# Kernel optimization log

Measured on AMD Instinct MI355X. Metric: run time of the kernel, lower is better.

Reference implementation:

```python
import jax, jax.numpy as jnp
import numpy as np

EMBED_DIM = 1024
NUM_HEADS = 16
HEAD_DIM = EMBED_DIM // NUM_HEADS
ROPE_BASE = 10000.0


def setup_inputs() -> dict:
    key = jax.random.key(0)
    k1, k2, k3, k4, k5 = jax.random.split(key, 5)
    b, t = 4, 2048
    s = 1.0 / np.sqrt(EMBED_DIM)
    return {
        "query": jax.random.normal(k1, (b, t, EMBED_DIM), jnp.float32),
        "in_proj_w": jax.random.normal(k2, (3 * EMBED_DIM, EMBED_DIM), jnp.float32) * s,
        "in_proj_b": jax.random.normal(k3, (3 * EMBED_DIM,), jnp.float32) * 0.02,
        "out_proj_w": jax.random.normal(k4, (EMBED_DIM, EMBED_DIM), jnp.float32) * s,
        "out_proj_b": jax.random.normal(k5, (EMBED_DIM,), jnp.float32) * 0.02,
    }


def _rope_cos_sin(t: int, dtype):
    inv_freq = 1.0 / (ROPE_BASE ** (jnp.arange(0, HEAD_DIM, 2, dtype=jnp.float32) / HEAD_DIM))
    freqs = jnp.arange(t, dtype=jnp.float32)[:, None] * inv_freq[None, :]  # [t, hd/2]
    return jnp.cos(freqs).astype(dtype), jnp.sin(freqs).astype(dtype)


def _apply_rotary(x, cos, sin):
    # x: [b, h, t, hd]; cos/sin: [t, hd/2]
    x1 = x[..., ::2]
    x2 = x[..., 1::2]
    c = cos[None, None, :, :]
    s = sin[None, None, :, :]
    rotated = jnp.stack((x1 * c - x2 * s, x1 * s + x2 * c), axis=-1)  # [b,h,t,hd/2,2]
    return rotated.reshape(x.shape)


def reference(query, in_proj_w, in_proj_b, out_proj_w, out_proj_b):
    b, t, d = query.shape
    qkv = query @ in_proj_w.T + in_proj_b  # [b, t, 3d]
    q, k, v = jnp.split(qkv, 3, axis=-1)
    def heads(x):
        return x.reshape(b, t, NUM_HEADS, HEAD_DIM).transpose(0, 2, 1, 3)  # [b,h,t,hd]
    q, k, v = heads(q), heads(k), heads(v)
    cos, sin = _rope_cos_sin(t, query.dtype)
    q = _apply_rotary(q, cos, sin)
    k = _apply_rotary(k, cos, sin)
    scale = 1.0 / np.sqrt(HEAD_DIM)
    scores = jnp.einsum('bhqd,bhkd->bhqk', q, k) * scale  # [b,h,t,t]
    probs = jax.nn.softmax(scores, axis=-1)
    attn = jnp.einsum('bhqk,bhkd->bhqd', probs, v)
    out = attn.transpose(0, 2, 1, 3).reshape(b, t, d)
    return out @ out_proj_w.T + out_proj_b
```

## Files before the change

kernel.cpp:

```cpp
#include <hip/hip_runtime.h>
#include <hip/hip_bf16.h>

#define EMBED 1024
#define NHEADS 16
#define HDIM 64
#define BATCH 4
#define SEQ 2048
#define BT (BATCH*SEQ)
#define NQKV (3*EMBED)


typedef _Float16 f16;
typedef __attribute__((ext_vector_type(8))) _Float16 half8;
typedef __attribute__((ext_vector_type(4))) _Float16 half4;
typedef __attribute__((ext_vector_type(4))) float f32x4;
typedef __attribute__((ext_vector_type(16))) float f32x16;
typedef __attribute__((ext_vector_type(4))) unsigned int u32x4;

__device__ __forceinline__ f32x4 mfma16f(half8 a, half8 b, f32x4 c) {
    return __builtin_amdgcn_mfma_f32_16x16x32_f16(a, b, c, 0, 0, 0);
}
__device__ __forceinline__ f32x16 mfma32(half8 a, half8 b, f32x16 c) {
    return __builtin_amdgcn_mfma_f32_32x32x16_f16(a, b, c, 0, 0, 0);
}
__device__ __forceinline__ f32x16 z16() {
    f32x16 z;
    #pragma unroll
    for (int i = 0; i < 16; i++) z[i] = 0.f;
    return z;
}
__device__ __forceinline__ unsigned int pk16(float a, float b) {
    auto h = __builtin_amdgcn_cvt_pkrtz(a, b);
    return __builtin_bit_cast(unsigned int, h);
}
__device__ __forceinline__ half8 mk8(unsigned int w0, unsigned int w1,
                                     unsigned int w2, unsigned int w3) {
    u32x4 v = (u32x4){w0, w1, w2, w3};
    return __builtin_bit_cast(half8, v);
}
__device__ __forceinline__ void pswap(unsigned int &a, unsigned int &b) {
    asm("v_permlane32_swap_b32 %0, %1" : "+v"(a), "+v"(b));
}

__device__ __forceinline__ half8 cvt8(float4 a, float4 b) {
    half8 r;
    r[0] = (f16)a.x; r[1] = (f16)a.y; r[2] = (f16)a.z; r[3] = (f16)a.w;
    r[4] = (f16)b.x; r[5] = (f16)b.y; r[6] = (f16)b.z; r[7] = (f16)b.w;
    return r;
}

__device__ __forceinline__ void gload16(const void* g, void* l) {
    __builtin_amdgcn_global_load_lds(
        (const __attribute__((address_space(1))) void*)g,
        (__attribute__((address_space(3))) void*)l, 16, 0, 0);
}

__global__ __launch_bounds__(256) void cvt_kernel(
    const float* __restrict__ X, const float* __restrict__ W1,
    const float* __restrict__ W2, f16* __restrict__ Xh,
    f16* __restrict__ W1h, f16* __restrict__ W2h, float2* __restrict__ CSt)
{
    const int u0 = blockIdx.x * 256 + threadIdx.x;
    #pragma unroll
    for (int i = 0; i < 3; i++) {
        const size_t uu = (size_t)u0 + (size_t)i * 524288;
        const float* src; f16* dst; size_t off;
        if (uu < 1048576)      { src = X;  dst = Xh;  off = uu * 8; }
        else if (uu < 1441792) { src = W1; dst = W1h; off = (uu - 1048576) * 8; }
        else                   { src = W2; dst = W2h; off = (uu - 1441792) * 8; }
        float4 a = *(const float4*)(src + off);
        float4 b = *(const float4*)(src + off + 4);
        *(half8*)(dst + off) = cvt8(a, b);
    }
    if (u0 < SEQ * 32) {
        const int t = u0 >> 5, fi = u0 & 31;
        const float ang = (float)t * exp2f(-0.41524103f * (float)fi);
        CSt[u0] = make_float2(cosf(ang), sinf(ang));
    }
}

__global__ __launch_bounds__(256) void qkv_rope_kernel(
    const f16* __restrict__ Xh, const f16* __restrict__ Wh,
    const float* __restrict__ bias, const float2* __restrict__ CSt,
    f16* __restrict__ Qg, f16* __restrict__ Kg, f16* __restrict__ Vtg)
{
    __shared__ __align__(16) char smem[34816];
    f16* Ah = (f16*)smem;
    f16* Bh = (f16*)(smem + 16384);
    f16 (*Ep)[136] = (f16(*)[136])smem;

    const int tid = threadIdx.x;
    const int m0 = blockIdx.y * 128, n0 = blockIdx.x * 128;
    const int lane = tid & 63;
    const int wv = tid >> 6, wm = wv >> 1, wn = wv & 1;
    const int quad = lane >> 4, l15 = lane & 15;
    const int sw = (l15 & 7) << 4;

    const int srow  = tid >> 3;
    const int sslot = (tid & 7) ^ (srow & 7);
    const f16* asrc = Xh + (size_t)(m0 + srow) * EMBED + sslot * 8;
    const f16* bsrc = Wh + (size_t)(n0 + srow) * EMBED + sslot * 8;

    f32x4 acc[4][4];
    #pragma unroll
    for (int i = 0; i < 4; i++)
        #pragma unroll
        for (int j = 0; j < 4; j++) acc[i][j] = (f32x4){0.f,0.f,0.f,0.f};

    for (int k0 = 0; k0 < EMBED; k0 += 64) {
        #pragma unroll
        for (int i = 0; i < 4; i++) {
            gload16(asrc + (size_t)i*32*EMBED + k0, Ah + i*2048 + tid*8);
            gload16(bsrc + (size_t)i*32*EMBED + k0, Bh + i*2048 + tid*8);
        }
        __syncthreads();

        half8 bf[4][2];
        #pragma unroll
        for (int nj = 0; nj < 4; nj++) {
            const int rb = wn*64 + nj*16 + l15;
            bf[nj][0] = *(const half8*)((const char*)Bh + rb*128 + ((quad*16) ^ sw));
            bf[nj][1] = *(const half8*)((const char*)Bh + rb*128 + ((64 + quad*16) ^ sw));
        }
        #pragma unroll
        for (int mi = 0; mi < 4; mi++) {
            const int ra = wm*64 + mi*16 + l15;
            half8 a0 = *(const half8*)((const char*)Ah + ra*128 + ((quad*16) ^ sw));
            half8 a1 = *(const half8*)((const char*)Ah + ra*128 + ((64 + quad*16) ^ sw));
            #pragma unroll
            for (int nj = 0; nj < 4; nj++) {
                acc[mi][nj] = mfma16f(a0, bf[nj][0], acc[mi][nj]);
                acc[mi][nj] = mfma16f(a1, bf[nj][1], acc[mi][nj]);
            }
        }
        __syncthreads();
    }

    const int sect = n0 >> 10;
    const int h0   = (n0 & 1023) >> 6;
    const int bb   = m0 >> 11, t0 = m0 & 2047;

    #pragma unroll
    for (int mi = 0; mi < 4; mi++) {
        #pragma unroll
        for (int nj = 0; nj < 4; nj++) {
            const int ncol = wn*64 + nj*16 + l15;
            const int hd = ncol & 63;
            const float bz = bias[n0 + ncol];
            #pragma unroll
            for (int r = 0; r < 4; r++) {
                const int tl = wm*64 + mi*16 + quad*4 + r;
                float v = acc[mi][nj][r] + bz;
                if (sect < 2) {
                    float partner = __shfl_xor(v, 1, 64);
                    float2 cs2 = CSt[(t0 + tl)*32 + (hd >> 1)];
                    float o = (hd & 1) ? fmaf(partner, cs2.y, v * cs2.x)
                                       : fmaf(v, cs2.x, -(partner * cs2.y));
                    Ep[tl][ncol] = (f16)o;
                } else {
                    Ep[ncol][tl] = (f16)v;
                }
            }
        }
    }
    __syncthreads();

    const int orow = tid >> 1;
    const int oc   = (tid & 1) * 64;
    f16* dst;
    if (sect == 2) {
        const int h = h0 + (orow >> 6), d = orow & 63;
        dst = Vtg + ((size_t)((bb*NHEADS + h) * HDIM + d)) * SEQ + t0 + oc;
    } else {
        const int h = h0 + (tid & 1);
        f16* base = (sect == 0) ? Qg : Kg;
        dst = base + ((size_t)((bb*NHEADS + h) * SEQ + t0 + orow)) * HDIM;
    }
    #pragma unroll
    for (int c8 = 0; c8 < 8; c8++)
        *(half8*)(dst + c8*8) = *(const half8*)&Ep[orow][oc + c8*8];
}

__global__ __launch_bounds__(128, 2) void attn_kernel(
    const f16* __restrict__ Qg, const f16* __restrict__ Kg,
    const f16* __restrict__ Vtg, f16* __restrict__ Ow)
{
    __shared__ __align__(16) f16 KV[2][2][64*64];

    const int tid  = threadIdx.x;
    const int lane = tid & 63, wq = tid >> 6;
    const int hi   = lane >> 5, col = lane & 31;

    const int lin = blockIdx.y * 16 + blockIdx.x;
    const int bh  = (lin & 7) + ((lin >> 7) << 3);
    const int qb  = (lin >> 3) & 15;
    const int q0  = qb * 128;

    const f16* Kb = Kg  + (size_t)bh * SEQ * HDIM;
    const f16* Vb = Vtg + (size_t)bh * HDIM * SEQ;

    const int r8   = tid >> 3;
    const int slot = tid & 7;

    #pragma unroll
    for (int g = 0; g < 4; g++) {
        const int row = g*16 + r8;
        const int sc  = (slot ^ (row & 7)) * 8;
        gload16(Kb + (size_t)row * HDIM + sc, &KV[0][0][0] + g*1024 + tid*8);
        gload16(Vb + (size_t)row * SEQ  + sc, &KV[0][1][0] + g*1024 + tid*8);
    }

    half8 qf[2][4];
    #pragma unroll
    for (int nb = 0; nb < 2; nb++) {
        const f16* qsrc = Qg + (size_t)bh * SEQ * HDIM
                        + (size_t)(q0 + wq*64 + nb*32 + col) * HDIM + hi*8;
        #pragma unroll
        for (int kc = 0; kc < 4; kc++)
            qf[nb][kc] = *(const half8*)(qsrc + kc*16);
    }

    f32x16 oacc[2][2];
    oacc[0][0] = z16(); oacc[0][1] = z16();
    oacc[1][0] = z16(); oacc[1][1] = z16();
    float lsum[2] = {0.f, 0.f};

    __syncthreads();

    for (int it = 0; it < 32; it++) {
        const f16* kl = &KV[it & 1][0][0];
        const f16* vl = &KV[it & 1][1][0];

        if (it < 31) {
            f16* kd = &KV[(it + 1) & 1][0][0];
            f16* vd = &KV[(it + 1) & 1][1][0];
            const int j0n = (it + 1) * 64;
            #pragma unroll
            for (int g = 0; g < 4; g++) {
                const int row = g*16 + r8;
                const int sc  = (slot ^ (row & 7)) * 8;
                gload16(Kb + (size_t)(j0n + row) * HDIM + sc, kd + g*1024 + tid*8);
                gload16(Vb + (size_t)row * SEQ + j0n + sc,    vd + g*1024 + tid*8);
            }
        }

        half8 kf[2][4];
        #pragma unroll
        for (int jb = 0; jb < 2; jb++) {
            const int row = jb*32 + col;
            const char* base = (const char*)kl + row*128;
            const int sz = (row & 7) << 4;
            #pragma unroll
            for (int kc = 0; kc < 4; kc++)
                kf[jb][kc] = *(const half8*)(base + ((kc*32 + hi*16) ^ sz));
        }

        unsigned int pw[2][4][4];
        #pragma unroll
        for (int nb = 0; nb < 2; nb++) {
            f32x16 s0 = z16(), s1 = z16();
            __builtin_amdgcn_s_setprio(1);
            #pragma unroll
            for (int kc = 0; kc < 4; kc++) s0 = mfma32(kf[0][kc], qf[nb][kc], s0);
            #pragma unroll
            for (int kc = 0; kc < 4; kc++) s1 = mfma32(kf[1][kc], qf[nb][kc], s1);
            __builtin_amdgcn_s_setprio(0);

            float e0[16], e1[16];
            #pragma unroll
            for (int r = 0; r < 16; r++) {
                e0[r] = __expf(fmaf(s0[r], 0.125f, -4.0f));
                e1[r] = __expf(fmaf(s1[r], 0.125f, -4.0f));
            }
            float t00 = (e0[0]+e0[1]) + (e0[2]+e0[3]);
            float t01 = (e0[4]+e0[5]) + (e0[6]+e0[7]);
            float t02 = (e0[8]+e0[9]) + (e0[10]+e0[11]);
            float t03 = (e0[12]+e0[13]) + (e0[14]+e0[15]);
            float t10 = (e1[0]+e1[1]) + (e1[2]+e1[3]);
            float t11 = (e1[4]+e1[5]) + (e1[6]+e1[7]);
            float t12 = (e1[8]+e1[9]) + (e1[10]+e1[11]);
            float t13 = (e1[12]+e1[13]) + (e1[14]+e1[15]);
            lsum[nb] += ((t00+t01)+(t02+t03)) + ((t10+t11)+(t12+t13));

            unsigned int a, b;
            a = pk16(e0[0],  e0[1]);  b = pk16(e0[4],  e0[5]);
            pswap(a, b); pw[nb][0][0] = a; pw[nb][0][2] = b;
            a = pk16(e0[2],  e0[3]);  b = pk16(e0[6],  e0[7]);
            pswap(a, b); pw[nb][0][1] = a; pw[nb][0][3] = b;
            a = pk16(e0[8],  e0[9]);  b = pk16(e0[12], e0[13]);
            pswap(a, b); pw[nb][1][0] = a; pw[nb][1][2] = b;
            a = pk16(e0[10], e0[11]); b = pk16(e0[14], e0[15]);
            pswap(a, b); pw[nb][1][1] = a; pw[nb][1][3] = b;

            a = pk16(e1[0],  e1[1]);  b = pk16(e1[4],  e1[5]);
            pswap(a, b); pw[nb][2][0] = a; pw[nb][2][2] = b;
            a = pk16(e1[2],  e1[3]);  b = pk16(e1[6],  e1[7]);
            pswap(a, b); pw[nb][2][1] = a; pw[nb][2][3] = b;
            a = pk16(e1[8],  e1[9]);  b = pk16(e1[12], e1[13]);
            pswap(a, b); pw[nb][3][0] = a; pw[nb][3][2] = b;
            a = pk16(e1[10], e1[11]); b = pk16(e1[14], e1[15]);
            pswap(a, b); pw[nb][3][1] = a; pw[nb][3][3] = b;
        }

        __builtin_amdgcn_s_setprio(1);
        #pragma unroll
        for (int kc2 = 0; kc2 < 4; kc2++) {
            half8 pb0 = mk8(pw[0][kc2][0], pw[0][kc2][1], pw[0][kc2][2], pw[0][kc2][3]);
            half8 pb1 = mk8(pw[1][kc2][0], pw[1][kc2][1], pw[1][kc2][2], pw[1][kc2][3]);
            #pragma unroll
            for (int db = 0; db < 2; db++) {
                const int row = db*32 + col;
                const int sz = (row & 7) << 4;
                half8 vf = *(const half8*)((const char*)vl + row*128
                                           + ((kc2*32 + hi*16) ^ sz));
                oacc[db][0] = mfma32(vf, pb0, oacc[db][0]);
                oacc[db][1] = mfma32(vf, pb1, oacc[db][1]);
            }
        }
        __builtin_amdgcn_s_setprio(0);

        __syncthreads();
    }

    float invl[2];
    invl[0] = 1.0f / (lsum[0] + __shfl_xor(lsum[0], 32, 64));
    invl[1] = 1.0f / (lsum[1] + __shfl_xor(lsum[1], 32, 64));

    const int bb = bh >> 4, h = bh & 15;
    #pragma unroll
    for (int nb = 0; nb < 2; nb++) {
        const int t = q0 + wq*64 + nb*32 + col;
        f16* od = Ow + (size_t)(bb*SEQ + t) * EMBED + h*HDIM + hi*4;
        #pragma unroll
        for (int db = 0; db < 2; db++) {
            #pragma unroll
            for (int rg = 0; rg < 4; rg++) {
                half4 o;
                o[0] = (f16)(oacc[db][nb][rg*4+0] * invl[nb]);
                o[1] = (f16)(oacc[db][nb][rg*4+1] * invl[nb]);
                o[2] = (f16)(oacc[db][nb][rg*4+2] * invl[nb]);
                o[3] = (f16)(oacc[db][nb][rg*4+3] * invl[nb]);
                *(half4*)(od + db*32 + rg*8) = o;
            }
        }
    }
}

__global__ __launch_bounds__(256) void outproj_kernel(
    const f16* __restrict__ Aw, const f16* __restrict__ Wh,
    const float* __restrict__ bias, float* __restrict__ Out)
{
    __shared__ __align__(16) char smem[32768];
    f16* Ah = (f16*)smem;
    f16* Bh = (f16*)(smem + 16384);

    const int tid = threadIdx.x;
    const int m0 = blockIdx.y * 128, n0 = blockIdx.x * 128;
    const int lane = tid & 63;
    const int wv = tid >> 6, wm = wv >> 1, wn = wv & 1;
    const int quad = lane >> 4, l15 = lane & 15;
    const int sw = (l15 & 7) << 4;

    const int srow  = tid >> 3;
    const int sslot = (tid & 7) ^ (srow & 7);
    const f16* asrc = Aw + (size_t)(m0 + srow) * EMBED + sslot * 8;
    const f16* bsrc = Wh + (size_t)(n0 + srow) * EMBED + sslot * 8;

    f32x4 acc[4][4];
    #pragma unroll
    for (int i = 0; i < 4; i++)
        #pragma unroll
        for (int j = 0; j < 4; j++) acc[i][j] = (f32x4){0.f,0.f,0.f,0.f};

    for (int k0 = 0; k0 < EMBED; k0 += 64) {
        #pragma unroll
        for (int i = 0; i < 4; i++) {
            gload16(asrc + (size_t)i*32*EMBED + k0, Ah + i*2048 + tid*8);
            gload16(bsrc + (size_t)i*32*EMBED + k0, Bh + i*2048 + tid*8);
        }
        __syncthreads();

        half8 bf[4][2];
        #pragma unroll
        for (int nj = 0; nj < 4; nj++) {
            const int rb = wn*64 + nj*16 + l15;
            bf[nj][0] = *(const half8*)((const char*)Bh + rb*128 + ((quad*16) ^ sw));
            bf[nj][1] = *(const half8*)((const char*)Bh + rb*128 + ((64 + quad*16) ^ sw));
        }
        #pragma unroll
        for (int mi = 0; mi < 4; mi++) {
            const int ra = wm*64 + mi*16 + l15;
            half8 a0 = *(const half8*)((const char*)Ah + ra*128 + ((quad*16) ^ sw));
            half8 a1 = *(const half8*)((const char*)Ah + ra*128 + ((64 + quad*16) ^ sw));
            #pragma unroll
            for (int nj = 0; nj < 4; nj++) {
                acc[mi][nj] = mfma16f(a0, bf[nj][0], acc[mi][nj]);
                acc[mi][nj] = mfma16f(a1, bf[nj][1], acc[mi][nj]);
            }
        }
        __syncthreads();
    }

    #pragma unroll
    for (int mi = 0; mi < 4; mi++) {
        #pragma unroll
        for (int nj = 0; nj < 4; nj++) {
            const int n = n0 + wn*64 + nj*16 + l15;
            const float bz = bias[n];
            #pragma unroll
            for (int r = 0; r < 4; r++) {
                const int m = m0 + wm*64 + mi*16 + quad*4 + r;
                Out[(size_t)m * EMBED + n] = acc[mi][nj][r] + bz;
            }
        }
    }
}

extern "C" void kernel_launch(void* const* d_in, const int* in_sizes, int n_in,
                              void* d_out, int out_size, void* d_ws, size_t ws_size,
                              hipStream_t stream)
{
    const float* query = (const float*)d_in[0];
    const float* in_w  = (const float*)d_in[1];
    const float* in_b  = (const float*)d_in[2];
    const float* out_w = (const float*)d_in[3];
    const float* out_b = (const float*)d_in[4];
    float* out = (float*)d_out;

    const size_t NT = (size_t)BATCH * NHEADS * SEQ * HDIM;
    char* ws = (char*)d_ws;
    f16* Qg  = (f16*)ws;
    f16* Kg  = (f16*)(ws + 2*NT);
    f16* Vtg = (f16*)(ws + 4*NT);
    f16* Aw  = (f16*)(ws + 6*NT);
    f16* Xh  = (f16*)(ws + 6*NT);
    f16* W1h = (f16*)(ws + 8*NT);
    f16* W2h = (f16*)(ws + 8*NT + 6291456);
    float2* CSt = (float2*)(ws + 8*NT + 6291456 + 2097152);

    cvt_kernel<<<2048, 256, 0, stream>>>(query, in_w, out_w, Xh, W1h, W2h, CSt);
    dim3 g1(NQKV / 128, BT / 128);
    qkv_rope_kernel<<<g1, 256, 0, stream>>>(Xh, W1h, in_b, CSt, Qg, Kg, Vtg);
    dim3 g2(SEQ / 128, BATCH * NHEADS);
    attn_kernel<<<g2, 128, 0, stream>>>(Qg, Kg, Vtg, Aw);
    dim3 g3(EMBED / 128, BT / 128);
    outproj_kernel<<<g3, 256, 0, stream>>>(Aw, W2h, out_b, out);
}
```

Before: 320.1 us.

## Double-buffer LDS in QKV and out-proj GEMMs and remap blocks across XCDs

Both GEMM kernels now keep two LDS stages and issue the global-to-LDS loads for the next K tile before computing on the current one, so memory latency overlaps with MFMA work. Block indices are also remapped so consecutive tiles spread across the 8 XCDs, grouping neighbouring tiles per die for L2 reuse. The cost is 64KB of LDS per block, which lowers occupancy. The hunk that would close each loop iteration is not visible, so the synchronisation between buffers cannot be checked.

```diff
diff --git a/kernel.cpp b/kernel.cpp
--- a/kernel.cpp
+++ b/kernel.cpp
@@ -84,13 +84,20 @@
     const float* __restrict__ bias, const float2* __restrict__ CSt,
     f16* __restrict__ Qg, f16* __restrict__ Kg, f16* __restrict__ Vtg)
 {
-    __shared__ __align__(16) char smem[34816];
-    f16* Ah = (f16*)smem;
-    f16* Bh = (f16*)(smem + 16384);
+    __shared__ __align__(16) char smem[65536];
+    f16* A0 = (f16*)smem;
+    f16* B0 = (f16*)(smem + 16384);
+    f16* A1 = (f16*)(smem + 32768);
+    f16* B1 = (f16*)(smem + 49152);
     f16 (*Ep)[136] = (f16(*)[136])smem;
 
     const int tid = threadIdx.x;
-    const int m0 = blockIdx.y * 128, n0 = blockIdx.x * 128;
+
+    const int L   = blockIdx.y * 24 + blockIdx.x;
+    const int nw  = (L & 7) * 192 + (L >> 3);
+    const int m0  = (nw / 24) * 128;
+    const int n0  = (nw % 24) * 128;
+
     const int lane = tid & 63;
     const int wv = tid >> 6, wm = wv >> 1, wn = wv & 1;
     const int quad = lane >> 4, l15 = lane & 15;
@@ -107,26 +114,39 @@
         #pragma unroll
         for (int j = 0; j < 4; j++) acc[i][j] = (f32x4){0.f,0.f,0.f,0.f};
 
-    for (int k0 = 0; k0 < EMBED; k0 += 64) {
-        #pragma unroll
-        for (int i = 0; i < 4; i++) {
-            gload16(asrc + (size_t)i*32*EMBED + k0, Ah + i*2048 + tid*8);
-            gload16(bsrc + (size_t)i*32*EMBED + k0, Bh + i*2048 + tid*8);
-        }
-        __syncthreads();
+    #pragma unroll
+    for (int i = 0; i < 4; i++) {
+        gload16(asrc + (size_t)i*32*EMBED, A0 + i*2048 + tid*8);
+        gload16(bsrc + (size_t)i*32*EMBED, B0 + i*2048 + tid*8);
+    }
+    __syncthreads();
+
+    for (int t = 0; t < 16; t++) {
+        const f16* Ac = (t & 1) ? A1 : A0;
+        const f16* Bc = (t & 1) ? B1 : B0;
+        if (t < 15) {
+            f16* An = (t & 1) ? A0 : A1;
+            f16* Bn = (t & 1) ? B0 : B1;
+            const int k0 = (t + 1) * 64;
+            #pragma unroll
+            for (int i = 0; i < 4; i++) {
+                gload16(asrc + (size_t)i*32*EMBED + k0, An + i*2048 + tid*8);
+                gload16(bsrc + (size_t)i*32*EMBED + k0, Bn + i*2048 + tid*8);
+            }
+        }
 
         half8 bf[4][2];
         #pragma unroll
         for (int nj = 0; nj < 4; nj++) {
             const int rb = wn*64 + nj*16 + l15;
-            bf[nj][0] = *(const half8*)((const char*)Bh + rb*128 + ((quad*16) ^ sw));
-            bf[nj][1] = *(const half8*)((const char*)Bh + rb*128 + ((64 + quad*16) ^ sw));
+            bf[nj][0] = *(const half8*)((const char*)Bc + rb*128 + ((quad*16) ^ sw));
+            bf[nj][1] = *(const half8*)((const char*)Bc + rb*128 + ((64 + quad*16) ^ sw));
         }
         #pragma unroll
         for (int mi = 0; mi < 4; mi++) {
             const int ra = wm*64 + mi*16 + l15;
-            half8 a0 = *(const half8*)((const char*)Ah + ra*128 + ((quad*16) ^ sw));
-            half8 a1 = *(const half8*)((const char*)Ah + ra*128 + ((64 + quad*16) ^ sw));
+            half8 a0 = *(const half8*)((const char*)Ac + ra*128 + ((quad*16) ^ sw));
+            half8 a1 = *(const half8*)((const char*)Ac + ra*128 + ((64 + quad*16) ^ sw));
             #pragma unroll
             for (int nj = 0; nj < 4; nj++) {
                 acc[mi][nj] = mfma16f(a0, bf[nj][0], acc[mi][nj]);
@@ -350,12 +370,19 @@
     const f16* __restrict__ Aw, const f16* __restrict__ Wh,
     const float* __restrict__ bias, float* __restrict__ Out)
 {
-    __shared__ __align__(16) char smem[32768];
-    f16* Ah = (f16*)smem;
-    f16* Bh = (f16*)(smem + 16384);
+    __shared__ __align__(16) char smem[65536];
+    f16* A0 = (f16*)smem;
+    f16* B0 = (f16*)(smem + 16384);
+    f16* A1 = (f16*)(smem + 32768);
+    f16* B1 = (f16*)(smem + 49152);
 
     const int tid = threadIdx.x;
-    const int m0 = blockIdx.y * 128, n0 = blockIdx.x * 128;
+
+    const int L   = blockIdx.y * 8 + blockIdx.x;
+    const int nw  = (L & 7) * 64 + (L >> 3);
+    const int m0  = (nw / 8) * 128;
+    const int n0  = (nw % 8) * 128;
+
     const int lane = tid & 63;
     const int wv = tid >> 6, wm = wv >> 1, wn = wv & 1;
     const int quad = lane >> 4, l15 = lane & 15;
@@ -372,26 +399,39 @@
         #pragma unroll
         for (int j = 0; j < 4; j++) acc[i][j] = (f32x4){0.f,0.f,0.f,0.f};
 
-    for (int k0 = 0; k0 < EMBED; k0 += 64) {
-        #pragma unroll
-        for (int i = 0; i < 4; i++) {
-            gload16(asrc + (size_t)i*32*EMBED + k0, Ah + i*2048 + tid*8);
-            gload16(bsrc + (size_t)i*32*EMBED + k0, Bh + i*2048 + tid*8);
-        }
-        __syncthreads();
+    #pragma unroll
+    for (int i = 0; i < 4; i++) {
+        gload16(asrc + (size_t)i*32*EMBED, A0 + i*2048 + tid*8);
+        gload16(bsrc + (size_t)i*32*EMBED, B0 + i*2048 + tid*8);
+    }
+    __syncthreads();
+
+    for (int t = 0; t < 16; t++) {
+        const f16* Ac = (t & 1) ? A1 : A0;
+        const f16* Bc = (t & 1) ? B1 : B0;
+        if (t < 15) {
+            f16* An = (t & 1) ? A0 : A1;
+            f16* Bn = (t & 1) ? B0 : B1;
+            const int k0 = (t + 1) * 64;
+            #pragma unroll
+            for (int i = 0; i < 4; i++) {
+                gload16(asrc + (size_t)i*32*EMBED + k0, An + i*2048 + tid*8);
+                gload16(bsrc + (size_t)i*32*EMBED + k0, Bn + i*2048 + tid*8);
+            }
+        }
 
         half8 bf[4][2];
         #pragma unroll
         for (int nj = 0; nj < 4; nj++) {
             const int rb = wn*64 + nj*16 + l15;
-            bf[nj][0] = *(const half8*)((const char*)Bh + rb*128 + ((quad*16) ^ sw));
-            bf[nj][1] = *(const half8*)((const char*)Bh + rb*128 + ((64 + quad*16) ^ sw));
+            bf[nj][0] = *(const half8*)((const char*)Bc + rb*128 + ((quad*16) ^ sw));
+            bf[nj][1] = *(const half8*)((const char*)Bc + rb*128 + ((64 + quad*16) ^ sw));
         }
         #pragma unroll
         for (int mi = 0; mi < 4; mi++) {
             const int ra = wm*64 + mi*16 + l15;
-            half8 a0 = *(const half8*)((const char*)Ah + ra*128 + ((quad*16) ^ sw));
-            half8 a1 = *(const half8*)((const char*)Ah + ra*128 + ((64 + quad*16) ^ sw));
+            half8 a0 = *(const half8*)((const char*)Ac + ra*128 + ((quad*16) ^ sw));
+            half8 a1 = *(const half8*)((const char*)Ac + ra*128 + ((64 + quad*16) ^ sw));
             #pragma unroll
             for (int nj = 0; nj < 4; nj++) {
                 acc[mi][nj] = mfma16f(a0, bf[nj][0], acc[mi][nj]);
```

Measured after the change: 332.4 us. +3.8%, slower.
